# Kernel tuning notes

Measured on AMD Instinct MI355X. Metric: run time of the kernel, lower is better.

## Reference

```python
import jax, jax.numpy as jnp
import numpy as np

B, S, E, H = 4, 1024, 2048, 16
D = E // H  # head_dim = 128


def setup_inputs() -> dict:
    key = jax.random.key(0)
    k1, k2, k3, k4, k5 = jax.random.split(key, 5)
    scale = 1.0 / np.sqrt(E)
    return {
        "query": jax.random.normal(k1, (B, S, E), dtype=jnp.float32),
        "in_proj_weight": jax.random.normal(k2, (3 * E, E), dtype=jnp.float32) * scale,
        "in_proj_bias": jax.random.normal(k3, (3 * E,), dtype=jnp.float32) * 0.02,
        "out_proj_weight": jax.random.normal(k4, (E, E), dtype=jnp.float32) * scale,
        "out_proj_bias": jax.random.normal(k5, (E,), dtype=jnp.float32) * 0.02,
    }


def reference(query, in_proj_weight, in_proj_bias, out_proj_weight, out_proj_bias):
    b, s, e = query.shape
    d = e // H
    # fused QKV projection: [B,S,3E]
    proj = jnp.einsum("bse,fe->bsf", query, in_proj_weight) + in_proj_bias
    q, k, v = jnp.split(proj, 3, axis=-1)
    # [B,S,E] -> [B,H,S,D]
    def to_heads(t):
        return t.reshape(b, s, H, d).transpose(0, 2, 1, 3)
    q, k, v = to_heads(q), to_heads(k), to_heads(v)
    # scaled dot-product attention (non-causal, no mask, no dropout)
    scores = jnp.einsum("bhqd,bhkd->bhqk", q, k) / jnp.sqrt(jnp.asarray(d, q.dtype))
    attn = jax.nn.softmax(scores, axis=-1)
    ctx = jnp.einsum("bhqk,bhkd->bhqd", attn, v)
    # [B,H,S,D] -> [B,S,E]
    ctx = ctx.transpose(0, 2, 1, 3).reshape(b, s, e)
    out = jnp.einsum("bse,fe->bsf", ctx, out_proj_weight) + out_proj_bias
    return out
```

## Files before the change

kernel.cpp:

```cpp
#include <hip/hip_runtime.h>
#include <hip/hip_fp16.h>

#define F16 _Float16
typedef F16 f16x8 __attribute__((ext_vector_type(8)));
typedef F16 f16x4 __attribute__((ext_vector_type(4)));
typedef float f32x4 __attribute__((ext_vector_type(4)));

__global__ void cvt_f32_f16(const float* __restrict__ src, F16* __restrict__ dst, int n) {
    int idx = blockIdx.x * blockDim.x + threadIdx.x;
    int stride = gridDim.x * blockDim.x;
    for (int i = idx * 4; i < n; i += stride * 4) {
        float4 v = *reinterpret_cast<const float4*>(src + i);
        f16x4 o;
        o[0] = (F16)v.x; o[1] = (F16)v.y; o[2] = (F16)v.z; o[3] = (F16)v.w;
        *reinterpret_cast<f16x4*>(dst + i) = o;
    }
}

__device__ __forceinline__ void gl_lds16(const F16* g, F16* l) {
    __builtin_amdgcn_global_load_lds(
        (const __attribute__((address_space(1))) void*)g,
        (__attribute__((address_space(3))) void*)l, 16, 0, 0);
}

template <int EPI>
__global__ __launch_bounds__(256, 2) void gemm_nt(
    const F16* __restrict__ A, const F16* __restrict__ Bw, const float* __restrict__ bias,
    F16* __restrict__ q_ws, F16* __restrict__ k_ws, F16* __restrict__ v_ws,
    float* __restrict__ fout, int M, int N, int K)
{
    __shared__ __align__(16) F16 lds[2][2][4096];
    const int tid = threadIdx.x;
    const int w = tid >> 6, l = tid & 63;
    const int lr = l & 15, lg = l >> 4;
    const int nbm = M >> 7;
    const int mb = blockIdx.x % nbm;
    const int nb = blockIdx.x / nbm;
    const long brow = (long)mb * 128;
    const long bcol = (long)nb * 128;
    const int wr = w >> 1, wc = w & 1;

    f32x4 acc[4][4];
#pragma unroll
    for (int i = 0; i < 4; ++i)
#pragma unroll
        for (int j = 0; j < 4; ++j) acc[i][j] = f32x4{0.f, 0.f, 0.f, 0.f};

    const F16* Abase = A + brow * K;
    const F16* Bbase = Bw + bcol * K;

    auto stage = [&](int buf, int kt) {
        const int k0 = kt << 5;
#pragma unroll
        for (int i = 0; i < 2; ++i) {
            const int rb = (i * 256 + tid) >> 6;
            const F16* sa = Abase + (long)(rb * 16 + lr) * K + k0 + lg * 8;
            gl_lds16(sa, &lds[buf][0][(i * 256 + w * 64) * 8]);
        }
#pragma unroll
        for (int i = 0; i < 2; ++i) {
            const int rb = (i * 256 + tid) >> 6;
            const F16* sb = Bbase + (long)(rb * 16 + lr) * K + k0 + lg * 8;
            gl_lds16(sb, &lds[buf][1][(i * 256 + w * 64) * 8]);
        }
    };

    const int nk = K >> 5;
    stage(0, 0);
    __syncthreads();
    int cur = 0;
    for (int kt = 0; kt < nk; ++kt) {
        if (kt + 1 < nk) stage(cur ^ 1, kt + 1);
        f16x8 af[4], bf[4];
#pragma unroll
        for (int mi = 0; mi < 4; ++mi)
            af[mi] = *reinterpret_cast<const f16x8*>(&lds[cur][0][((wr * 4 + mi) * 64 + l) * 8]);
#pragma unroll
        for (int ni = 0; ni < 4; ++ni)
            bf[ni] = *reinterpret_cast<const f16x8*>(&lds[cur][1][((wc * 4 + ni) * 64 + l) * 8]);
#pragma unroll
        for (int mi = 0; mi < 4; ++mi)
#pragma unroll
            for (int ni = 0; ni < 4; ++ni)
                acc[mi][ni] = __builtin_amdgcn_mfma_f32_16x16x32_f16(af[mi], bf[ni], acc[mi][ni], 0, 0, 0);
        __syncthreads();
        cur ^= 1;
    }

    const int r0 = wr * 64 + lg * 4;
    const int c0 = wc * 64 + lr;
    if constexpr (EPI == 0) {
        const int part = (int)(bcol >> 11);
        const int hh = ((int)bcol >> 7) & 15;
        const int bI = (int)(brow >> 10);
        const int s_base = ((int)brow & 1023) + r0;
#pragma unroll
        for (int mi = 0; mi < 4; ++mi) {
#pragma unroll
            for (int ni = 0; ni < 4; ++ni) {
                const int d = c0 + ni * 16;
                const float bv = bias[bcol + d];
                if (part == 2) {
                    f16x4 pv;
#pragma unroll
                    for (int r = 0; r < 4; ++r) pv[r] = (F16)(acc[mi][ni][r] + bv);
                    const int s0 = s_base + mi * 16;
                    F16* dst = v_ws + ((long)((bI * 16 + hh) * 128 + d)) * 1024 + s0;
                    *reinterpret_cast<f16x4*>(dst) = pv;
                } else {
                    F16* base = (part == 0) ? q_ws : k_ws;
                    const float scl = (part == 0) ? 0.08838834764831845f : 1.0f;
#pragma unroll
                    for (int r = 0; r < 4; ++r) {
                        const int s = s_base + mi * 16 + r;
                        base[((long)((bI * 16 + hh) * 1024 + s)) * 128 + d] =
                            (F16)((acc[mi][ni][r] + bv) * scl);
                    }
                }
            }
        }
    } else {
#pragma unroll
        for (int mi = 0; mi < 4; ++mi)
#pragma unroll
            for (int ni = 0; ni < 4; ++ni) {
                const long row = brow + r0 + mi * 16;
                const long col = bcol + c0 + ni * 16;
                const float bv = bias[col];
#pragma unroll
                for (int r = 0; r < 4; ++r)
                    fout[(row + r) * N + col] = acc[mi][ni][r] + bv;
            }
    }
}

__global__ __launch_bounds__(256, 2) void attn_kernel(
    const F16* __restrict__ q_ws, const F16* __restrict__ k_ws,
    const F16* __restrict__ v_ws, F16* __restrict__ ctx)
{
    __shared__ __align__(16) F16 kt[2][64 * 128];
    __shared__ __align__(16) F16 vt[2][128 * 64];
    __shared__ __align__(16) F16 p_lds[4][2048];
    const int tid = threadIdx.x;
    const int w = tid >> 6, l = tid & 63;
    const int lr = l & 15, lg = l >> 4;
    const int work = (blockIdx.x & 7) * 64 + (blockIdx.x >> 3);
    const int bh = work >> 3, qt = work & 7;
    const int b = bh >> 4, h = bh & 15;
    const int q0 = qt * 128 + w * 32;

    const F16* kbh = k_ws + (long)bh * 1024 * 128;
    const F16* vbh = v_ws + (long)bh * 128 * 1024;

    f16x8 qf[2][4];
#pragma unroll
    for (int mi = 0; mi < 2; ++mi)
#pragma unroll
        for (int ks = 0; ks < 4; ++ks)
            qf[mi][ks] = *reinterpret_cast<const f16x8*>(
                q_ws + ((long)bh * 1024 + q0 + mi * 16 + lr) * 128 + ks * 32 + lg * 8);

    auto stage = [&](int buf, int kv0) {
#pragma unroll
        for (int t = 0; t < 4; ++t) {
            const int chunk = t * 256 + tid;
            const int row = chunk >> 4;
            const int colb = (chunk & 15) << 4;
            const int gcol = colb ^ ((row & 7) << 4);
            gl_lds16(kbh + (long)(kv0 + row) * 128 + (gcol >> 1),
                     &kt[buf][(t * 256 + w * 64) * 8]);
        }
#pragma unroll
        for (int t = 0; t < 4; ++t) {
            const int chunk = t * 256 + tid;
            const int d = chunk >> 3;
            const int colb = (chunk & 7) << 4;
            const int gcol = colb ^ ((d & 7) << 4);
            gl_lds16(vbh + (long)d * 1024 + kv0 + (gcol >> 1),
                     &vt[buf][(t * 256 + w * 64) * 8]);
        }
    };

    float mrun[2][4], lsum[2][4];
#pragma unroll
    for (int mi = 0; mi < 2; ++mi)
#pragma unroll
        for (int r = 0; r < 4; ++r) { mrun[mi][r] = -1e30f; lsum[mi][r] = 0.f; }
    f32x4 acc[2][8];
#pragma unroll
    for (int mi = 0; mi < 2; ++mi)
#pragma unroll
        for (int nf = 0; nf < 8; ++nf) acc[mi][nf] = f32x4{0.f, 0.f, 0.f, 0.f};

    stage(0, 0);
    __syncthreads();
    int cur = 0;
    for (int it = 0; it < 16; ++it) {
        if (it + 1 < 16) stage(cur ^ 1, (it + 1) * 64);

        f32x4 sc[2][4];
#pragma unroll
        for (int mi = 0; mi < 2; ++mi)
#pragma unroll
            for (int cf = 0; cf < 4; ++cf) sc[mi][cf] = f32x4{0.f, 0.f, 0.f, 0.f};
#pragma unroll
        for (int cf = 0; cf < 4; ++cf) {
#pragma unroll
            for (int ks = 0; ks < 4; ++ks) {
                const int row = cf * 16 + lr;
                const int eff = (ks * 64 + lg * 16) ^ ((row & 7) << 4);
                f16x8 kf = *reinterpret_cast<const f16x8*>(&kt[cur][row * 128 + (eff >> 1)]);
#pragma unroll
                for (int mi = 0; mi < 2; ++mi)
                    sc[mi][cf] = __builtin_amdgcn_mfma_f32_16x16x32_f16(qf[mi][ks], kf, sc[mi][cf], 0, 0, 0);
            }
        }

#pragma unroll
        for (int mi = 0; mi < 2; ++mi) {
            float t4[4];
#pragma unroll
            for (int r = 0; r < 4; ++r)
                t4[r] = fmaxf(fmaxf(sc[mi][0][r], sc[mi][1][r]), fmaxf(sc[mi][2][r], sc[mi][3][r]));
#pragma unroll
            for (int msk = 1; msk < 16; msk <<= 1)
#pragma unroll
                for (int r = 0; r < 4; ++r) t4[r] = fmaxf(t4[r], __shfl_xor(t4[r], msk));
            float al[4], rs[4], p[4][4];
#pragma unroll
            for (int r = 0; r < 4; ++r) {
                const float mn = fmaxf(mrun[mi][r], t4[r]);
                al[r] = __expf(mrun[mi][r] - mn);
                mrun[mi][r] = mn;
#pragma unroll
                for (int cf = 0; cf < 4; ++cf) p[cf][r] = __expf(sc[mi][cf][r] - mn);
                rs[r] = (p[0][r] + p[1][r]) + (p[2][r] + p[3][r]);
            }
#pragma unroll
            for (int msk = 1; msk < 16; msk <<= 1)
#pragma unroll
                for (int r = 0; r < 4; ++r) rs[r] += __shfl_xor(rs[r], msk);
#pragma unroll
            for (int r = 0; r < 4; ++r) lsum[mi][r] = lsum[mi][r] * al[r] + rs[r];
#pragma unroll
            for (int nf = 0; nf < 8; ++nf)
#pragma unroll
                for (int r = 0; r < 4; ++r) acc[mi][nf][r] *= al[r];
#pragma unroll
            for (int cf = 0; cf < 4; ++cf)
#pragma unroll
                for (int r = 0; r < 4; ++r) {
                    const int chunk = (mi * 2 + (cf >> 1)) * 64 + (lg * 4 + r) + ((cf & 1) * 2 + (lr >> 3)) * 16;
                    p_lds[w][chunk * 8 + (lr & 7)] = (F16)p[cf][r];
                }
        }

        f16x8 pf[2][2];
#pragma unroll
        for (int mi = 0; mi < 2; ++mi)
#pragma unroll
            for (int half = 0; half < 2; ++half)
                pf[mi][half] = *reinterpret_cast<const f16x8*>(&p_lds[w][((mi * 2 + half) * 64 + l) * 8]);
#pragma unroll
        for (int nf = 0; nf < 8; ++nf) {
#pragma unroll
            for (int half = 0; half < 2; ++half) {
                const int d = nf * 16 + lr;
                const int eff = (half * 64 + lg * 16) ^ ((d & 7) << 4);
                f16x8 vf = *reinterpret_cast<const f16x8*>(&vt[cur][d * 64 + (eff >> 1)]);
#pragma unroll
                for (int mi = 0; mi < 2; ++mi)
                    acc[mi][nf] = __builtin_amdgcn_mfma_f32_16x16x32_f16(pf[mi][half], vf, acc[mi][nf], 0, 0, 0);
            }
        }
        __syncthreads();
        cur ^= 1;
    }

#pragma unroll
    for (int mi = 0; mi < 2; ++mi) {
        float inv[4];
#pragma unroll
        for (int r = 0; r < 4; ++r) inv[r] = 1.f / lsum[mi][r];
#pragma unroll
        for (int nf = 0; nf < 8; ++nf)
#pragma unroll
            for (int r = 0; r < 4; ++r) {
                const int s = q0 + mi * 16 + lg * 4 + r;
                const int e = h * 128 + nf * 16 + lr;
                ctx[((long)(b * 1024 + s)) * 2048 + e] = (F16)(acc[mi][nf][r] * inv[r]);
            }
    }
}

extern "C" void kernel_launch(void* const* d_in, const int* in_sizes, int n_in,
                              void* d_out, int out_size, void* d_ws, size_t ws_size,
                              hipStream_t stream) {
    const float* query = (const float*)d_in[0];
    const float* w_in  = (const float*)d_in[1];
    const float* b_in  = (const float*)d_in[2];
    const float* w_out = (const float*)d_in[3];
    const float* b_out = (const float*)d_in[4];
    float* out = (float*)d_out;

    char* ws = (char*)d_ws;
    size_t off = 0;
    auto carve = [&](size_t bytes) -> void* {
        void* p = ws + off;
        off += (bytes + 255) & ~(size_t)255;
        return p;
    };
    F16* xq  = (F16*)carve(8388608ULL * 2);
    F16* wih = (F16*)carve(12582912ULL * 2);
    F16* woh = (F16*)carve(4194304ULL * 2);
    F16* qws = (F16*)carve(8388608ULL * 2);
    F16* kws = (F16*)carve(8388608ULL * 2);
    F16* vws = (F16*)carve(8388608ULL * 2);
    F16* ctx = (F16*)carve(8388608ULL * 2);

    cvt_f32_f16<<<1024, 256, 0, stream>>>(query, xq, 8388608);
    cvt_f32_f16<<<1024, 256, 0, stream>>>(w_in, wih, 12582912);
    cvt_f32_f16<<<512, 256, 0, stream>>>(w_out, woh, 4194304);

    gemm_nt<0><<<32 * 48, 256, 0, stream>>>(xq, wih, b_in, qws, kws, vws, nullptr, 4096, 6144, 2048);
    attn_kernel<<<512, 256, 0, stream>>>(qws, kws, vws, ctx);
    gemm_nt<1><<<32 * 16, 256, 0, stream>>>(ctx, woh, b_out, nullptr, nullptr, nullptr, out, 4096, 2048, 2048);
}
```

Measured before the change: 455.6 us.

## Replace GEMM with 256x256-tile 8-wave kernel using staggered async loads

Replaces the 128x128 tile, 4-wave GEMM with a 256x256 tile, 8-wave kernel that uses a K-step of 64. The new kernel splits each LDS tile into halves whose global-to-LDS loads are issued ahead, interleaved across four compute phases, and waited on with explicit vmcnt, barriers and priority hints. It also remaps block ids into an XCD-aware order. The aim is more operand reuse per byte loaded and better overlap of memory traffic with MFMA work. In exchange it uses 128 KB of LDS per block, which limits occupancy, and launches far fewer blocks: 384 for the QKV GEMM and 128 for the output GEMM, possibly below the CU count.

```diff
diff --git a/kernel.cpp b/kernel.cpp
--- a/kernel.cpp
+++ b/kernel.cpp
@@ -24,113 +24,154 @@
 }
 
 template <int EPI>
-__global__ __launch_bounds__(256, 2) void gemm_nt(
+__global__ __launch_bounds__(512, 2) void gemm8(
     const F16* __restrict__ A, const F16* __restrict__ Bw, const float* __restrict__ bias,
     F16* __restrict__ q_ws, F16* __restrict__ k_ws, F16* __restrict__ v_ws,
     float* __restrict__ fout, int M, int N, int K)
 {
-    __shared__ __align__(16) F16 lds[2][2][4096];
+    __shared__ __align__(16) F16 lds[2][4][8192];
     const int tid = threadIdx.x;
     const int w = tid >> 6, l = tid & 63;
     const int lr = l & 15, lg = l >> 4;
-    const int nbm = M >> 7;
-    const int mb = blockIdx.x % nbm;
-    const int nb = blockIdx.x / nbm;
-    const long brow = (long)mb * 128;
-    const long bcol = (long)nb * 128;
-    const int wr = w >> 1, wc = w & 1;
-
-    f32x4 acc[4][4];
-#pragma unroll
-    for (int i = 0; i < 4; ++i)
-#pragma unroll
-        for (int j = 0; j < 4; ++j) acc[i][j] = f32x4{0.f, 0.f, 0.f, 0.f};
-
-    const F16* Abase = A + brow * K;
-    const F16* Bbase = Bw + bcol * K;
-
-    auto stage = [&](int buf, int kt) {
-        const int k0 = kt << 5;
-#pragma unroll
-        for (int i = 0; i < 2; ++i) {
-            const int rb = (i * 256 + tid) >> 6;
-            const F16* sa = Abase + (long)(rb * 16 + lr) * K + k0 + lg * 8;
-            gl_lds16(sa, &lds[buf][0][(i * 256 + w * 64) * 8]);
-        }
-#pragma unroll
-        for (int i = 0; i < 2; ++i) {
-            const int rb = (i * 256 + tid) >> 6;
-            const F16* sb = Bbase + (long)(rb * 16 + lr) * K + k0 + lg * 8;
-            gl_lds16(sb, &lds[buf][1][(i * 256 + w * 64) * 8]);
-        }
-    };
-
-    const int nk = K >> 5;
-    stage(0, 0);
-    __syncthreads();
-    int cur = 0;
-    for (int kt = 0; kt < nk; ++kt) {
-        if (kt + 1 < nk) stage(cur ^ 1, kt + 1);
-        f16x8 af[4], bf[4];
-#pragma unroll
-        for (int mi = 0; mi < 4; ++mi)
-            af[mi] = *reinterpret_cast<const f16x8*>(&lds[cur][0][((wr * 4 + mi) * 64 + l) * 8]);
-#pragma unroll
-        for (int ni = 0; ni < 4; ++ni)
-            bf[ni] = *reinterpret_cast<const f16x8*>(&lds[cur][1][((wc * 4 + ni) * 64 + l) * 8]);
-#pragma unroll
-        for (int mi = 0; mi < 4; ++mi)
-#pragma unroll
-            for (int ni = 0; ni < 4; ++ni)
-                acc[mi][ni] = __builtin_amdgcn_mfma_f32_16x16x32_f16(af[mi], bf[ni], acc[mi][ni], 0, 0, 0);
-        __syncthreads();
-        cur ^= 1;
-    }
-
-    const int r0 = wr * 64 + lg * 4;
-    const int c0 = wc * 64 + lr;
+    const int wm = w >> 2, wn = w & 3;
+
+    const int nbn = N >> 8;
+    const int cpx = (int)gridDim.x >> 3;
+    const int work = ((int)blockIdx.x & 7) * cpx + ((int)blockIdx.x >> 3);
+    const int nb = work % nbn, mb = work / nbn;
+    const long brow = (long)mb * 256, bcol = (long)nb * 256;
+
+    const F16* rb0 = A + brow * K;
+    const F16* rb1 = rb0 + 128 * (long)K;
+    const F16* rb2 = Bw + bcol * K;
+    const F16* rb3 = rb2 + 128 * (long)K;
+
+    const int sr0 = ((tid >> 7) << 4) + (tid & 15);
+    const int skk = (((tid >> 6) & 1) << 5) + (((tid >> 4) & 3) << 3);
+    const int wb8 = (w << 6) * 8;
+
+#define GISSUE(BUF, R, S, KT, RB) \
+    gl_lds16(RB + (long)(sr0 + S * 64) * K + (KT) * 64 + skk, \
+             &lds[BUF][R][S * 4096 + wb8])
+
+    const int NK = K >> 6;
+
+    f32x4 acc[8][4];
+#pragma unroll
+    for (int f = 0; f < 8; ++f)
+#pragma unroll
+        for (int nf = 0; nf < 4; ++nf) acc[f][nf] = f32x4{0.f, 0.f, 0.f, 0.f};
+
+    GISSUE(0, 0, 0, 0, rb0); GISSUE(0, 0, 1, 0, rb0);
+    GISSUE(0, 1, 0, 0, rb1); GISSUE(0, 1, 1, 0, rb1);
+    GISSUE(0, 2, 0, 0, rb2); GISSUE(0, 2, 1, 0, rb2);
+    GISSUE(0, 3, 0, 0, rb3); GISSUE(0, 3, 1, 0, rb3);
+    if (NK > 1) {
+        GISSUE(1, 2, 0, 1, rb2); GISSUE(1, 2, 1, 1, rb2);
+        GISSUE(1, 3, 0, 1, rb3); GISSUE(1, 3, 1, 1, rb3);
+        GISSUE(1, 0, 0, 1, rb0); GISSUE(1, 1, 0, 1, rb1);
+        asm volatile("s_waitcnt vmcnt(6)" ::: "memory");
+    } else {
+        asm volatile("s_waitcnt vmcnt(0)" ::: "memory");
+    }
+    __builtin_amdgcn_s_barrier();
+
+    for (int kt = 0; kt < NK; ++kt) {
+        const int cur = kt & 1, nxt = cur ^ 1;
+        const F16* Areg = &lds[cur][wm][0];
+        const F16* Breg = &lds[cur][2 + (wn >> 1)][0];
+        f16x8 b[4][2];
+#pragma unroll
+        for (int nf = 0; nf < 4; ++nf)
+#pragma unroll
+            for (int ks = 0; ks < 2; ++ks)
+                b[nf][ks] = *reinterpret_cast<const f16x8*>(
+                    Breg + ((((wn & 1) * 4 + nf) * 2 + ks) * 64 + l) * 8);
+#pragma unroll
+        for (int p = 0; p < 4; ++p) {
+            f16x8 a[2][2];
+#pragma unroll
+            for (int mf = 0; mf < 2; ++mf)
+#pragma unroll
+                for (int ks = 0; ks < 2; ++ks)
+                    a[mf][ks] = *reinterpret_cast<const f16x8*>(
+                        Areg + (((2 * p + mf) * 2 + ks) * 64 + l) * 8);
+            if (p == 0) {
+                if (kt + 1 < NK) { GISSUE(nxt, 0, 1, kt + 1, rb0); GISSUE(nxt, 1, 1, kt + 1, rb1); }
+            } else if (p == 1) {
+                if (kt + 2 < NK) { GISSUE(cur, 2, 0, kt + 2, rb2); GISSUE(cur, 2, 1, kt + 2, rb2); }
+            } else if (p == 2) {
+                if (kt + 2 < NK) { GISSUE(cur, 3, 0, kt + 2, rb3); GISSUE(cur, 3, 1, kt + 2, rb3); }
+            } else {
+                if (kt + 2 < NK) { GISSUE(cur, 0, 0, kt + 2, rb0); GISSUE(cur, 1, 0, kt + 2, rb1); }
+            }
+            __builtin_amdgcn_sched_barrier(0);
+            __builtin_amdgcn_s_barrier();
+            asm volatile("s_waitcnt lgkmcnt(0)" ::: "memory");
+            __builtin_amdgcn_sched_barrier(0);
+            __builtin_amdgcn_s_setprio(1);
+#pragma unroll
+            for (int mf = 0; mf < 2; ++mf)
+#pragma unroll
+                for (int nf = 0; nf < 4; ++nf)
+#pragma unroll
+                    for (int ks = 0; ks < 2; ++ks)
+                        acc[2 * p + mf][nf] = __builtin_amdgcn_mfma_f32_16x16x32_f16(
+                            a[mf][ks], b[nf][ks], acc[2 * p + mf][nf], 0, 0, 0);
+            __builtin_amdgcn_s_setprio(0);
+            __builtin_amdgcn_sched_barrier(0);
+            if (p == 3) {
+                if (kt + 2 < NK) asm volatile("s_waitcnt vmcnt(6)" ::: "memory");
+                else             asm volatile("s_waitcnt vmcnt(0)" ::: "memory");
+            }
+            __builtin_amdgcn_s_barrier();
+        }
+    }
+#undef GISSUE
+
+    const int col0 = (int)bcol + wn * 64;
+    const int row0 = (int)brow + wm * 128;
     if constexpr (EPI == 0) {
         const int part = (int)(bcol >> 11);
-        const int hh = ((int)bcol >> 7) & 15;
-        const int bI = (int)(brow >> 10);
-        const int s_base = ((int)brow & 1023) + r0;
-#pragma unroll
-        for (int mi = 0; mi < 4; ++mi) {
-#pragma unroll
-            for (int ni = 0; ni < 4; ++ni) {
-                const int d = c0 + ni * 16;
-                const float bv = bias[bcol + d];
-                if (part == 2) {
+        const int bI = row0 >> 10;
+        const int sb = row0 & 1023;
+        const float scl = (part == 0) ? 0.08838834764831845f : 1.0f;
+#pragma unroll
+        for (int nf = 0; nf < 4; ++nf) {
+            const int gcol = col0 + nf * 16 + lr;
+            const float bv = bias[gcol];
+            const int d = gcol & 127;
+            const int hh = (gcol >> 7) & 15;
+            if (part == 2) {
+                F16* dst0 = v_ws + ((long)((bI * 16 + hh) * 128 + d)) * 1024;
+#pragma unroll
+                for (int f = 0; f < 8; ++f) {
                     f16x4 pv;
 #pragma unroll
-                    for (int r = 0; r < 4; ++r) pv[r] = (F16)(acc[mi][ni][r] + bv);
-                    const int s0 = s_base + mi * 16;
-                    F16* dst = v_ws + ((long)((bI * 16 + hh) * 128 + d)) * 1024 + s0;
-                    *reinterpret_cast<f16x4*>(dst) = pv;
-                } else {
-                    F16* base = (part == 0) ? q_ws : k_ws;
-                    const float scl = (part == 0) ? 0.08838834764831845f : 1.0f;
-#pragma unroll
-                    for (int r = 0; r < 4; ++r) {
-                        const int s = s_base + mi * 16 + r;
-                        base[((long)((bI * 16 + hh) * 1024 + s)) * 128 + d] =
-                            (F16)((acc[mi][ni][r] + bv) * scl);
-                    }
+                    for (int r = 0; r < 4; ++r) pv[r] = (F16)(acc[f][nf][r] + bv);
+                    *reinterpret_cast<f16x4*>(dst0 + sb + f * 16 + lg * 4) = pv;
                 }
+            } else {
+                F16* dst0 = ((part == 0) ? q_ws : k_ws) + ((long)(bI * 16 + hh) * 1024) * 128 + d;
+#pragma unroll
+                for (int f = 0; f < 8; ++f)
+#pragma unroll
+                    for (int r = 0; r < 4; ++r)
+                        dst0[(long)(sb + f * 16 + lg * 4 + r) * 128] =
+                            (F16)((acc[f][nf][r] + bv) * scl);
             }
         }
     } else {
 #pragma unroll
-        for (int mi = 0; mi < 4; ++mi)
-#pragma unroll
-            for (int ni = 0; ni < 4; ++ni) {
-                const long row = brow + r0 + mi * 16;
-                const long col = bcol + c0 + ni * 16;
-                const float bv = bias[col];
+        for (int nf = 0; nf < 4; ++nf) {
+            const int gcol = col0 + nf * 16 + lr;
+            const float bv = bias[gcol];
+#pragma unroll
+            for (int f = 0; f < 8; ++f)
 #pragma unroll
                 for (int r = 0; r < 4; ++r)
-                    fout[(row + r) * N + col] = acc[mi][ni][r] + bv;
-            }
+                    fout[(long)(row0 + f * 16 + lg * 4 + r) * N + gcol] = acc[f][nf][r] + bv;
+        }
     }
 }
 
@@ -322,7 +363,7 @@
     cvt_f32_f16<<<1024, 256, 0, stream>>>(w_in, wih, 12582912);
     cvt_f32_f16<<<512, 256, 0, stream>>>(w_out, woh, 4194304);
 
-    gemm_nt<0><<<32 * 48, 256, 0, stream>>>(xq, wih, b_in, qws, kws, vws, nullptr, 4096, 6144, 2048);
+    gemm8<0><<<384, 512, 0, stream>>>(xq, wih, b_in, qws, kws, vws, nullptr, 4096, 6144, 2048);
     attn_kernel<<<512, 256, 0, stream>>>(qws, kws, vws, ctx);
-    gemm_nt<1><<<32 * 16, 256, 0, stream>>>(ctx, woh, b_out, nullptr, nullptr, nullptr, out, 4096, 2048, 2048);
-}
+    gemm8<1><<<128, 512, 0, stream>>>(ctx, woh, b_out, nullptr, nullptr, nullptr, out, 4096, 2048, 2048);
+}
```

Measured after the change: 418.5 us. 8.1% less time.
